# Optimization experiments

Hardware: AMD Instinct MI355X
Metric: run time of the kernel (lower is better)

Reference implementation:

```python
import jax, jax.numpy as jnp
import numpy as np

N_HEAD = 8


def setup_inputs() -> dict:
    key = jax.random.key(0)
    k1, k2, k3 = jax.random.split(key, 3)
    B, D, L = 4, 1024, 2048  # channels-first: (batch, feature, seq)
    q = jax.random.normal(k1, (B, D, L), dtype=jnp.float32)
    k = jax.random.normal(k2, (B, D, L), dtype=jnp.float32)
    v = jax.random.normal(k3, (B, D, L), dtype=jnp.float32)
    gamma = jnp.ones((), dtype=jnp.float32)  # nn.Parameter scalar, init 1.0
    return {"q": q, "k": k, "v": v, "gamma": gamma}


def reference(q, k, v, gamma):
    # q, k, v: (B, D, L) channels-first. Head split on feature dim (-2).
    B, Dq, Lq = q.shape
    Dv, Lk = v.shape[-2], v.shape[-1]
    h = N_HEAD
    dq = Dq // h  # per-head query/key dim
    dv = Dv // h  # per-head value dim
    qh = q.reshape(B, h, dq, Lq)
    kh = k.reshape(B, h, dq, Lk)
    vh = v.reshape(B, h, dv, Lk)
    # scale = sqrt(q.size(-2)) AFTER head split, i.e. sqrt(d_head)
    scale = 1.0 / jnp.sqrt(jnp.asarray(dq, dtype=q.dtype))
    # qk: (B, h, Lq, Lk)
    qk = jnp.einsum('bhdq,bhdl->bhql', qh, kh) * scale
    sm = jax.nn.softmax(qk, axis=-1)
    # torch: (sm.unsqueeze(-3) * v.unsqueeze(-2)).sum(-1) == contraction over Lk
    ret = jnp.einsum('bhql,bhdl->bhdq', sm, vh)  # (B, h, dv, Lq)
    ret = ret.reshape(B, Dv, Lq)  # torch: ret.view(-1, v_shape[-2], q_shape[-1])
    return gamma * ret
```

## Files before the change

### kernel.cpp

```cpp
#include <hip/hip_runtime.h>

#define SEQ 2048
#define DHEAD 128
#define BK 32
#define NBH 32

typedef __attribute__((ext_vector_type(8))) short bf16x8;
typedef __attribute__((ext_vector_type(8))) unsigned short us8;
typedef __attribute__((ext_vector_type(4))) float f32x4;

__device__ __forceinline__ unsigned short f2bf(float f) {
    unsigned u = __builtin_bit_cast(unsigned, f);
    u += 0x7fffu + ((u >> 16) & 1u);
    return (unsigned short)(u >> 16);
}

__device__ __forceinline__ void gload16(const unsigned short* g, unsigned short* l) {
    __builtin_amdgcn_global_load_lds((const __attribute__((address_space(1))) void*)g,
                                     (__attribute__((address_space(3))) void*)l, 16, 0, 0);
}

__global__ __launch_bounds__(256)
void tcvt_kernel(const float* __restrict__ in, unsigned short* __restrict__ outp,
                 float scl, int swz) {
    __shared__ __align__(16) unsigned short tile[64][136];
    const int tid = threadIdx.x;
    const int bh = blockIdx.x & 31;
    const int l0 = (blockIdx.x >> 5) * 64;
    const float* ip = in + (size_t)bh * DHEAD * SEQ;
    unsigned short* opx = outp + ((size_t)bh * SEQ + l0) * DHEAD;
    const int l = tid & 63;
    const int d0 = tid >> 6;
    for (int i = 0; i < 32; ++i) {
        int d = i * 4 + d0;
        tile[l][d] = f2bf(ip[(size_t)d * SEQ + l0 + l] * scl);
    }
    __syncthreads();
    const int lw = tid >> 2;
    const int cw = tid & 3;
    for (int j = 0; j < 4; ++j) {
        int pc = j * 4 + cw;
        int lc = swz ? (pc ^ (lw & 7)) : pc;
        bf16x8 d = *(const bf16x8*)&tile[lw][lc * 8];
        *(bf16x8*)&opx[(size_t)lw * DHEAD + pc * 8] = d;
    }
}

__global__ __launch_bounds__(256)
void vcvt_kernel(const float* __restrict__ in, unsigned short* __restrict__ outp) {
    size_t f = ((size_t)blockIdx.x * 256 + threadIdx.x) * 8;
    int bh  = (int)(f >> 18);
    int rem = (int)(f & 262143);
    int kt  = rem >> 12;
    int r2  = rem & 4095;
    int dv  = r2 >> 5;
    int e0  = r2 & 31;
    const float* src = in + ((size_t)bh * DHEAD + dv) * SEQ + kt * BK + e0;
    float4 a = *(const float4*)src;
    float4 b = *(const float4*)(src + 4);
    us8 r;
    r[0] = f2bf(a.x); r[1] = f2bf(a.y); r[2] = f2bf(a.z); r[3] = f2bf(a.w);
    r[4] = f2bf(b.x); r[5] = f2bf(b.y); r[6] = f2bf(b.z); r[7] = f2bf(b.w);
    *(us8*)(outp + f) = r;
}

__global__ __launch_bounds__(256, 2)
void attn_main(const unsigned short* __restrict__ qT,
               const unsigned short* __restrict__ kTg,
               const unsigned short* __restrict__ vW,
               const float* __restrict__ gamma,
               float* __restrict__ out) {
    __shared__ __align__(16) unsigned short kS[BK * DHEAD];
    __shared__ __align__(16) unsigned short vS[DHEAD * BK];
    __shared__ __align__(16) unsigned short pS[4][16][40];

    const int tid  = threadIdx.x;
    const int wv   = tid >> 6;
    const int lane = tid & 63;
    const int c    = lane & 15;
    const int quad = lane >> 4;

    const int bh  = blockIdx.x & 31;
    const int qlb = blockIdx.x >> 5;
    const size_t base = (size_t)bh * SEQ * DHEAD;

    const unsigned short* qb = qT + base;
    const unsigned short* kb = kTg + base;
    const unsigned short* vb = vW + base;
    float* op = out + base;

    const int ql0 = qlb * 128 + wv * 32;

    bf16x8 qf[2][4];
    for (int rs = 0; rs < 2; ++rs) {
        const unsigned short* qr = qb + (size_t)(ql0 + rs * 16 + c) * DHEAD;
        for (int s = 0; s < 4; ++s)
            qf[rs][s] = *(const bf16x8*)(qr + s * 32 + quad * 8);
    }

    f32x4 accO[2][8];
    for (int rs = 0; rs < 2; ++rs)
        for (int t = 0; t < 8; ++t)
            accO[rs][t] = (f32x4){0.f, 0.f, 0.f, 0.f};
    float lp[2][4] = {{0.f,0.f,0.f,0.f},{0.f,0.f,0.f,0.f}};

    const int ksw = c & 7;

    for (int kt = 0; kt < SEQ / BK; ++kt) {
        const int kl0 = kt * BK;
        __syncthreads();
        {
            const unsigned short* kg = kb + (size_t)kl0 * DHEAD;
            gload16(kg + tid * 8,           &kS[tid * 8]);
            gload16(kg + (tid + 256) * 8,   &kS[(tid + 256) * 8]);
            const unsigned short* vg = vb + (size_t)kt * (DHEAD * BK);
            gload16(vg + tid * 8,           &vS[tid * 8]);
            gload16(vg + (tid + 256) * 8,   &vS[(tid + 256) * 8]);
        }
        __syncthreads();

        bf16x8 vf[8];
        for (int t = 0; t < 8; ++t)
            vf[t] = *(const bf16x8*)&vS[(t * 16 + c) * BK + quad * 8];

        for (int rs = 0; rs < 2; ++rs) {
            f32x4 s0 = (f32x4){0.f,0.f,0.f,0.f};
            f32x4 s1 = (f32x4){0.f,0.f,0.f,0.f};
            for (int s = 0; s < 4; ++s) {
                int pc = (4 * s + quad) ^ ksw;
                bf16x8 b0 = *(const bf16x8*)&kS[c * DHEAD + pc * 8];
                bf16x8 b1 = *(const bf16x8*)&kS[(16 + c) * DHEAD + pc * 8];
                s0 = __builtin_amdgcn_mfma_f32_16x16x32_bf16(qf[rs][s], b0, s0, 0, 0, 0);
                s1 = __builtin_amdgcn_mfma_f32_16x16x32_bf16(qf[rs][s], b1, s1, 0, 0, 0);
            }

            float p0[4], p1[4];
            for (int r = 0; r < 4; ++r) {
                p0[r] = exp2f(s0[r]);
                p1[r] = exp2f(s1[r]);
                lp[rs][r] += p0[r] + p1[r];
                pS[wv][4 * quad + r][c]      = f2bf(p0[r]);
                pS[wv][4 * quad + r][16 + c] = f2bf(p1[r]);
            }
            asm volatile("s_waitcnt lgkmcnt(0)" ::: "memory");

            bf16x8 bp = *(const bf16x8*)&pS[wv][c][quad * 8];
            for (int t = 0; t < 8; ++t)
                accO[rs][t] = __builtin_amdgcn_mfma_f32_16x16x32_bf16(vf[t], bp, accO[rs][t], 0, 0, 0);
        }
    }

    const float gm = gamma[0];
    for (int rs = 0; rs < 2; ++rs) {
        float L[4];
        for (int r = 0; r < 4; ++r) {
            float s = lp[rs][r];
            s += __shfl_xor(s, 1, 16);
            s += __shfl_xor(s, 2, 16);
            s += __shfl_xor(s, 4, 16);
            s += __shfl_xor(s, 8, 16);
            L[r] = s;
        }
        int srcl = (c >> 2) << 4;
        float L0 = __shfl(L[0], srcl);
        float L1 = __shfl(L[1], srcl);
        float L2 = __shfl(L[2], srcl);
        float L3 = __shfl(L[3], srcl);
        int rsel = c & 3;
        float lsel = rsel == 0 ? L0 : rsel == 1 ? L1 : rsel == 2 ? L2 : L3;
        float sc = gm / lsel;
        int ql = ql0 + rs * 16 + c;
        for (int t = 0; t < 8; ++t)
            for (int r = 0; r < 4; ++r)
                op[(size_t)(t * 16 + quad * 4 + r) * SEQ + ql] = accO[rs][t][r] * sc;
    }
}

extern "C" void kernel_launch(void* const* d_in, const int* in_sizes, int n_in,
                              void* d_out, int out_size, void* d_ws, size_t ws_size,
                              hipStream_t stream) {
    (void)in_sizes; (void)n_in; (void)out_size; (void)ws_size;
    const float* q = (const float*)d_in[0];
    const float* k = (const float*)d_in[1];
    const float* v = (const float*)d_in[2];
    const float* g = (const float*)d_in[3];
    float* out = (float*)d_out;

    const size_t PER_T = (size_t)NBH * SEQ * DHEAD;
    unsigned short* qws = (unsigned short*)d_ws;
    unsigned short* kws = qws + PER_T;
    unsigned short* vws = kws + PER_T;

    const float SCL = 0.08838834764831845f * 1.44269504088896340f;

    tcvt_kernel<<<dim3(1024), dim3(256), 0, stream>>>(q, qws, SCL, 0);
    tcvt_kernel<<<dim3(1024), dim3(256), 0, stream>>>(k, kws, 1.0f, 1);
    vcvt_kernel<<<dim3(4096), dim3(256), 0, stream>>>(v, vws);
    attn_main<<<dim3(512), dim3(256), 0, stream>>>(qws, kws, vws, g, out);
}
```

Measured before the change: 256.2 us.

## Double-buffer K/V tiles, merge conversion kernels, load Q directly in attention

Merges the K and V bf16 conversion kernels into a single launch and drops the separate Q conversion, so the attention kernel reads fp32 Q with strided loads and converts it in registers. The attention kernel now double-buffers K/V tiles in LDS, prefetching the next tile while computing the current one, which removes one barrier per iteration. It halves the query rows per block and raises the occupancy hint so twice as many blocks run. It also XOR-swizzles the V layout and reworks the K transpose staging to reduce LDS bank conflicts. The cost is uncoalesced strided Q reads and more LDS per block.

```diff
diff --git a/kernel.cpp b/kernel.cpp
--- a/kernel.cpp
+++ b/kernel.cpp
@@ -6,7 +6,6 @@
 #define NBH 32
 
 typedef __attribute__((ext_vector_type(8))) short bf16x8;
-typedef __attribute__((ext_vector_type(8))) unsigned short us8;
 typedef __attribute__((ext_vector_type(4))) float f32x4;
 
 __device__ __forceinline__ unsigned short f2bf(float f) {
@@ -21,58 +20,63 @@
 }
 
 __global__ __launch_bounds__(256)
-void tcvt_kernel(const float* __restrict__ in, unsigned short* __restrict__ outp,
-                 float scl, int swz) {
-    __shared__ __align__(16) unsigned short tile[64][136];
+void cvt_kernel(const float* __restrict__ kin, const float* __restrict__ vin,
+                unsigned short* __restrict__ kout, unsigned short* __restrict__ vout) {
     const int tid = threadIdx.x;
-    const int bh = blockIdx.x & 31;
-    const int l0 = (blockIdx.x >> 5) * 64;
-    const float* ip = in + (size_t)bh * DHEAD * SEQ;
-    unsigned short* opx = outp + ((size_t)bh * SEQ + l0) * DHEAD;
-    const int l = tid & 63;
-    const int d0 = tid >> 6;
-    for (int i = 0; i < 32; ++i) {
-        int d = i * 4 + d0;
-        tile[l][d] = f2bf(ip[(size_t)d * SEQ + l0 + l] * scl);
-    }
-    __syncthreads();
-    const int lw = tid >> 2;
-    const int cw = tid & 3;
-    for (int j = 0; j < 4; ++j) {
-        int pc = j * 4 + cw;
-        int lc = swz ? (pc ^ (lw & 7)) : pc;
-        bf16x8 d = *(const bf16x8*)&tile[lw][lc * 8];
-        *(bf16x8*)&opx[(size_t)lw * DHEAD + pc * 8] = d;
-    }
-}
-
-__global__ __launch_bounds__(256)
-void vcvt_kernel(const float* __restrict__ in, unsigned short* __restrict__ outp) {
-    size_t f = ((size_t)blockIdx.x * 256 + threadIdx.x) * 8;
-    int bh  = (int)(f >> 18);
-    int rem = (int)(f & 262143);
-    int kt  = rem >> 12;
-    int r2  = rem & 4095;
-    int dv  = r2 >> 5;
-    int e0  = r2 & 31;
-    const float* src = in + ((size_t)bh * DHEAD + dv) * SEQ + kt * BK + e0;
-    float4 a = *(const float4*)src;
-    float4 b = *(const float4*)(src + 4);
-    us8 r;
-    r[0] = f2bf(a.x); r[1] = f2bf(a.y); r[2] = f2bf(a.z); r[3] = f2bf(a.w);
-    r[4] = f2bf(b.x); r[5] = f2bf(b.y); r[6] = f2bf(b.z); r[7] = f2bf(b.w);
-    *(us8*)(outp + f) = r;
-}
-
-__global__ __launch_bounds__(256, 2)
-void attn_main(const unsigned short* __restrict__ qT,
+    if (blockIdx.x < 1024) {
+        __shared__ unsigned short tileT[DHEAD][66];
+        const int bh = blockIdx.x & 31;
+        const int l0 = (blockIdx.x >> 5) * 64;
+        const float* ip = kin + (size_t)bh * DHEAD * SEQ;
+        unsigned short* opx = kout + ((size_t)bh * SEQ + l0) * DHEAD;
+        const int l4 = (tid & 15) * 4;
+        const int dq = tid >> 4;
+        for (int pass = 0; pass < 8; ++pass) {
+            int d = pass * 16 + dq;
+            float4 f = *(const float4*)&ip[(size_t)d * SEQ + l0 + l4];
+            unsigned lo = (unsigned)f2bf(f.x) | ((unsigned)f2bf(f.y) << 16);
+            unsigned hi = (unsigned)f2bf(f.z) | ((unsigned)f2bf(f.w) << 16);
+            *(unsigned*)&tileT[d][l4]     = lo;
+            *(unsigned*)&tileT[d][l4 + 2] = hi;
+        }
+        __syncthreads();
+        const int lw = tid >> 2;
+        const int cw = tid & 3;
+        for (int j = 0; j < 4; ++j) {
+            int pc = j * 4 + cw;
+            int lc = pc ^ (lw & 7);
+            unsigned short tmp[8];
+            for (int k2 = 0; k2 < 8; ++k2) tmp[k2] = tileT[lc * 8 + k2][lw];
+            *(bf16x8*)&opx[(size_t)lw * DHEAD + pc * 8] = *(bf16x8*)tmp;
+        }
+    } else {
+        size_t f = ((size_t)(blockIdx.x - 1024) * 256 + tid) * 8;
+        int bh  = (int)(f >> 18);
+        int rem = (int)(f & 262143);
+        int kt  = rem >> 12;
+        int r2  = rem & 4095;
+        int dv  = r2 >> 5;
+        int e0  = r2 & 31;
+        const float* src = vin + ((size_t)bh * DHEAD + dv) * SEQ + kt * BK + e0;
+        float4 a = *(const float4*)src;
+        float4 b = *(const float4*)(src + 4);
+        unsigned short r[8] = {f2bf(a.x), f2bf(a.y), f2bf(a.z), f2bf(a.w),
+                               f2bf(b.x), f2bf(b.y), f2bf(b.z), f2bf(b.w)};
+        int pc = (e0 >> 3) ^ ((dv >> 1) & 3);
+        size_t off = ((size_t)bh * (SEQ / BK) + kt) * (DHEAD * BK) + dv * BK + pc * 8;
+        *(bf16x8*)&vout[off] = *(bf16x8*)r;
+    }
+}
+
+__global__ __launch_bounds__(256, 4)
+void attn_main(const float* __restrict__ q,
                const unsigned short* __restrict__ kTg,
                const unsigned short* __restrict__ vW,
                const float* __restrict__ gamma,
                float* __restrict__ out) {
-    __shared__ __align__(16) unsigned short kS[BK * DHEAD];
-    __shared__ __align__(16) unsigned short vS[DHEAD * BK];
-    __shared__ __align__(16) unsigned short pS[4][16][40];
+    __shared__ unsigned short kS[2][BK * DHEAD];
+    __shared__ unsigned short vS[2][DHEAD * BK];
+    __shared__ unsigned short pS[4][16][40];
 
     const int tid  = threadIdx.x;
     const int wv   = tid >> 6;
@@ -84,96 +88,104 @@
     const int qlb = blockIdx.x >> 5;
     const size_t base = (size_t)bh * SEQ * DHEAD;
 
-    const unsigned short* qb = qT + base;
+    const float* qp = q + base;
     const unsigned short* kb = kTg + base;
     const unsigned short* vb = vW + base;
     float* op = out + base;
 
-    const int ql0 = qlb * 128 + wv * 32;
-
-    bf16x8 qf[2][4];
-    for (int rs = 0; rs < 2; ++rs) {
-        const unsigned short* qr = qb + (size_t)(ql0 + rs * 16 + c) * DHEAD;
-        for (int s = 0; s < 4; ++s)
-            qf[rs][s] = *(const bf16x8*)(qr + s * 32 + quad * 8);
-    }
-
-    f32x4 accO[2][8];
-    for (int rs = 0; rs < 2; ++rs)
-        for (int t = 0; t < 8; ++t)
-            accO[rs][t] = (f32x4){0.f, 0.f, 0.f, 0.f};
-    float lp[2][4] = {{0.f,0.f,0.f,0.f},{0.f,0.f,0.f,0.f}};
+    const int ql0 = qlb * 64 + wv * 16;
+    const float SCL = 0.08838834764831845f * 1.44269504088896340f;
+
+    bf16x8 qf[4];
+    {
+        const int ql = ql0 + c;
+        for (int s = 0; s < 4; ++s) {
+            bf16x8 fqs;
+            for (int j = 0; j < 8; ++j)
+                fqs[j] = (short)f2bf(qp[(size_t)(s * 32 + quad * 8 + j) * SEQ + ql] * SCL);
+            qf[s] = fqs;
+        }
+    }
+
+    f32x4 accO[8];
+    for (int t = 0; t < 8; ++t) accO[t] = (f32x4){0.f, 0.f, 0.f, 0.f};
+    float lp[4] = {0.f, 0.f, 0.f, 0.f};
 
     const int ksw = c & 7;
+    const int vsw = (c >> 1) & 3;
+
+    {
+        const unsigned short* kg = kb;
+        gload16(kg + tid * 8,         &kS[0][tid * 8]);
+        gload16(kg + (tid + 256) * 8, &kS[0][(tid + 256) * 8]);
+        const unsigned short* vg = vb;
+        gload16(vg + tid * 8,         &vS[0][tid * 8]);
+        gload16(vg + (tid + 256) * 8, &vS[0][(tid + 256) * 8]);
+    }
 
     for (int kt = 0; kt < SEQ / BK; ++kt) {
-        const int kl0 = kt * BK;
+        const int cur = kt & 1;
         __syncthreads();
-        {
-            const unsigned short* kg = kb + (size_t)kl0 * DHEAD;
-            gload16(kg + tid * 8,           &kS[tid * 8]);
-            gload16(kg + (tid + 256) * 8,   &kS[(tid + 256) * 8]);
-            const unsigned short* vg = vb + (size_t)kt * (DHEAD * BK);
-            gload16(vg + tid * 8,           &vS[tid * 8]);
-            gload16(vg + (tid + 256) * 8,   &vS[(tid + 256) * 8]);
-        }
-        __syncthreads();
+
+        if (kt + 1 < SEQ / BK) {
+            const unsigned short* kg = kb + (size_t)(kt + 1) * (BK * DHEAD);
+            gload16(kg + tid * 8,         &kS[cur ^ 1][tid * 8]);
+            gload16(kg + (tid + 256) * 8, &kS[cur ^ 1][(tid + 256) * 8]);
+            const unsigned short* vg = vb + (size_t)(kt + 1) * (DHEAD * BK);
+            gload16(vg + tid * 8,         &vS[cur ^ 1][tid * 8]);
+            gload16(vg + (tid + 256) * 8, &vS[cur ^ 1][(tid + 256) * 8]);
+        }
 
         bf16x8 vf[8];
         for (int t = 0; t < 8; ++t)
-            vf[t] = *(const bf16x8*)&vS[(t * 16 + c) * BK + quad * 8];
-
-        for (int rs = 0; rs < 2; ++rs) {
-            f32x4 s0 = (f32x4){0.f,0.f,0.f,0.f};
-            f32x4 s1 = (f32x4){0.f,0.f,0.f,0.f};
-            for (int s = 0; s < 4; ++s) {
-                int pc = (4 * s + quad) ^ ksw;
-                bf16x8 b0 = *(const bf16x8*)&kS[c * DHEAD + pc * 8];
-                bf16x8 b1 = *(const bf16x8*)&kS[(16 + c) * DHEAD + pc * 8];
-                s0 = __builtin_amdgcn_mfma_f32_16x16x32_bf16(qf[rs][s], b0, s0, 0, 0, 0);
-                s1 = __builtin_amdgcn_mfma_f32_16x16x32_bf16(qf[rs][s], b1, s1, 0, 0, 0);
-            }
-
-            float p0[4], p1[4];
-            for (int r = 0; r < 4; ++r) {
-                p0[r] = exp2f(s0[r]);
-                p1[r] = exp2f(s1[r]);
-                lp[rs][r] += p0[r] + p1[r];
-                pS[wv][4 * quad + r][c]      = f2bf(p0[r]);
-                pS[wv][4 * quad + r][16 + c] = f2bf(p1[r]);
-            }
-            asm volatile("s_waitcnt lgkmcnt(0)" ::: "memory");
-
-            bf16x8 bp = *(const bf16x8*)&pS[wv][c][quad * 8];
-            for (int t = 0; t < 8; ++t)
-                accO[rs][t] = __builtin_amdgcn_mfma_f32_16x16x32_bf16(vf[t], bp, accO[rs][t], 0, 0, 0);
-        }
+            vf[t] = *(const bf16x8*)&vS[cur][(t * 16 + c) * BK + ((quad ^ vsw) * 8)];
+
+        f32x4 s0 = (f32x4){0.f, 0.f, 0.f, 0.f};
+        f32x4 s1 = (f32x4){0.f, 0.f, 0.f, 0.f};
+        for (int s = 0; s < 4; ++s) {
+            int pc = (4 * s + quad) ^ ksw;
+            bf16x8 b0 = *(const bf16x8*)&kS[cur][c * DHEAD + pc * 8];
+            bf16x8 b1 = *(const bf16x8*)&kS[cur][(16 + c) * DHEAD + pc * 8];
+            s0 = __builtin_amdgcn_mfma_f32_16x16x32_bf16(qf[s], b0, s0, 0, 0, 0);
+            s1 = __builtin_amdgcn_mfma_f32_16x16x32_bf16(qf[s], b1, s1, 0, 0, 0);
+        }
+
+        for (int r = 0; r < 4; ++r) {
+            float p0 = exp2f(s0[r]);
+            float p1 = exp2f(s1[r]);
+            lp[r] += p0 + p1;
+            pS[wv][4 * quad + r][c]      = f2bf(p0);
+            pS[wv][4 * quad + r][16 + c] = f2bf(p1);
+        }
+        asm volatile("s_waitcnt lgkmcnt(0)" ::: "memory");
+
+        bf16x8 bp = *(const bf16x8*)&pS[wv][c][quad * 8];
+        for (int t = 0; t < 8; ++t)
+            accO[t] = __builtin_amdgcn_mfma_f32_16x16x32_bf16(vf[t], bp, accO[t], 0, 0, 0);
     }
 
     const float gm = gamma[0];
-    for (int rs = 0; rs < 2; ++rs) {
-        float L[4];
-        for (int r = 0; r < 4; ++r) {
-            float s = lp[rs][r];
-            s += __shfl_xor(s, 1, 16);
-            s += __shfl_xor(s, 2, 16);
-            s += __shfl_xor(s, 4, 16);
-            s += __shfl_xor(s, 8, 16);
-            L[r] = s;
-        }
-        int srcl = (c >> 2) << 4;
-        float L0 = __shfl(L[0], srcl);
-        float L1 = __shfl(L[1], srcl);
-        float L2 = __shfl(L[2], srcl);
-        float L3 = __shfl(L[3], srcl);
-        int rsel = c & 3;
-        float lsel = rsel == 0 ? L0 : rsel == 1 ? L1 : rsel == 2 ? L2 : L3;
-        float sc = gm / lsel;
-        int ql = ql0 + rs * 16 + c;
-        for (int t = 0; t < 8; ++t)
-            for (int r = 0; r < 4; ++r)
-                op[(size_t)(t * 16 + quad * 4 + r) * SEQ + ql] = accO[rs][t][r] * sc;
-    }
+    float L[4];
+    for (int r = 0; r < 4; ++r) {
+        float s = lp[r];
+        s += __shfl_xor(s, 1, 16);
+        s += __shfl_xor(s, 2, 16);
+        s += __shfl_xor(s, 4, 16);
+        s += __shfl_xor(s, 8, 16);
+        L[r] = s;
+    }
+    int srcl = (c >> 2) << 4;
+    float L0 = __shfl(L[0], srcl);
+    float L1 = __shfl(L[1], srcl);
+    float L2 = __shfl(L[2], srcl);
+    float L3 = __shfl(L[3], srcl);
+    int rsel = c & 3;
+    float lsel = rsel == 0 ? L0 : rsel == 1 ? L1 : rsel == 2 ? L2 : L3;
+    float sc = gm / lsel;
+    int ql = ql0 + c;
+    for (int t = 0; t < 8; ++t)
+        for (int r = 0; r < 4; ++r)
+            op[(size_t)(t * 16 + quad * 4 + r) * SEQ + ql] = accO[t][r] * sc;
 }
 
 extern "C" void kernel_launch(void* const* d_in, const int* in_sizes, int n_in,
@@ -187,14 +199,9 @@
     float* out = (float*)d_out;
 
     const size_t PER_T = (size_t)NBH * SEQ * DHEAD;
-    unsigned short* qws = (unsigned short*)d_ws;
-    unsigned short* kws = qws + PER_T;
+    unsigned short* kws = (unsigned short*)d_ws;
     unsigned short* vws = kws + PER_T;
 
-    const float SCL = 0.08838834764831845f * 1.44269504088896340f;
-
-    tcvt_kernel<<<dim3(1024), dim3(256), 0, stream>>>(q, qws, SCL, 0);
-    tcvt_kernel<<<dim3(1024), dim3(256), 0, stream>>>(k, kws, 1.0f, 1);
-    vcvt_kernel<<<dim3(4096), dim3(256), 0, stream>>>(v, vws);
-    attn_main<<<dim3(512), dim3(256), 0, stream>>>(qws, kws, vws, g, out);
-}
+    cvt_kernel<<<dim3(1024 + 4096), dim3(256), 0, stream>>>(k, v, kws, vws);
+    attn_main<<<dim3(1024), dim3(256), 0, stream>>>(q, kws, vws, g, out);
+}
```

Result: faster. 232.6 us (-9.2%).
